# Optimization experiments

Hardware: AMD Instinct MI355X
Metric: run time of the kernel (lower is better)

## Reference

```python
import jax, jax.numpy as jnp
import numpy as np

C = 256
H = 8
D = C // H


def setup_inputs() -> dict:
    key = jax.random.key(0)
    ks = jax.random.split(key, 6)
    scale = 1.0 / np.sqrt(C)
    x = jax.random.normal(ks[0], (8, C, 2048), dtype=jnp.float32)
    Wq = jax.random.normal(ks[1], (C, C), dtype=jnp.float32) * scale
    Wk = jax.random.normal(ks[2], (C, C), dtype=jnp.float32) * scale
    Wv = jax.random.normal(ks[3], (C, C), dtype=jnp.float32) * scale
    Wo = jax.random.normal(ks[4], (C, C), dtype=jnp.float32) * scale
    bo = jax.random.normal(ks[5], (C,), dtype=jnp.float32) * 0.01
    return {"x": x, "Wq": Wq, "Wk": Wk, "Wv": Wv, "Wo": Wo, "bo": bo}


def reference(x, Wq, Wk, Wv, Wo, bo):
    # x: [N, C, L]; Conv1d(k=1) == per-position matmul with weight [out, in]
    q = jnp.einsum('oc,ncl->nol', Wq, x)
    k = jnp.einsum('oc,ncl->nol', Wk, x)
    v = jnp.einsum('oc,ncl->nol', Wv, x)
    N, _, L = x.shape
    # rearrange 'n (h d) l -> n l h d'
    q = q.reshape(N, H, D, L).transpose(0, 3, 1, 2)
    k = k.reshape(N, H, D, L).transpose(0, 3, 1, 2)
    v = v.reshape(N, H, D, L).transpose(0, 3, 1, 2)
    qk = jnp.einsum('nqhd,nkhd->nhqk', q, k)
    # NOTE: original scales by full embedding size (channels), not head_dim
    attn = jax.nn.softmax(qk * (C ** -0.5), axis=3)
    out = jnp.einsum('nhql,nlhd->nqhd', attn, v)
    # rearrange 'n l h d -> n (h d) l'
    out = out.transpose(0, 2, 3, 1).reshape(N, C, L)
    return jnp.einsum('oc,ncl->nol', Wo, out) + bo[None, :, None]
```

## Files before the change

### kernel.cpp

```cpp
#include <hip/hip_runtime.h>


typedef __bf16 bf8 __attribute__((ext_vector_type(8)));
typedef float f4 __attribute__((ext_vector_type(4)));
typedef float f32x4 __attribute__((ext_vector_type(4)));
typedef unsigned short u16;
typedef unsigned int u32;
typedef u16 u16x4 __attribute__((ext_vector_type(4)));
typedef u16 u16x8 __attribute__((ext_vector_type(8)));

__device__ __forceinline__ u16 f2bf(float f) {
  __bf16 h = (__bf16)f;
  return __builtin_bit_cast(u16, h);
}
__device__ __forceinline__ u32 pk2bf(float a, float b) {
  return ((u32)f2bf(b) << 16) | (u32)f2bf(a);
}
__device__ __forceinline__ u32 pktrunc(float a, float b) {
  return __builtin_amdgcn_perm(__builtin_bit_cast(u32, b),
                               __builtin_bit_cast(u32, a), 0x07060302u);
}
__device__ __forceinline__ float exp2_fast(float x) {
  return __builtin_amdgcn_exp2f(x);
}

#define MFMA(a, b, c) __builtin_amdgcn_mfma_f32_16x16x32_bf16((a), (b), (c), 0, 0, 0)

union bf8u { u32 u[4]; bf8 v; };
__device__ __forceinline__ bf8 mkbf8(u32 a, u32 b, u32 c, u32 d) {
  bf8u t; t.u[0] = a; t.u[1] = b; t.u[2] = c; t.u[3] = d; return t.v;
}
__device__ __forceinline__ bf8 ldw8(const float* p) {
  f32x4 u = *(const f32x4*)p;
  f32x4 v = *(const f32x4*)(p + 4);
  return mkbf8(pk2bf(u[0], u[1]), pk2bf(u[2], u[3]),
               pk2bf(v[0], v[1]), pk2bf(v[2], v[3]));
}

__global__ __launch_bounds__(256) void qkv_proj(
    const float* __restrict__ x, const float* __restrict__ Wq,
    const float* __restrict__ Wk, const float* __restrict__ Wv,
    u16* __restrict__ qbuf, u16* __restrict__ kbuf, u16* __restrict__ vbuf) {
  __shared__ __align__(16) u16 xt[64 * 264];
  const int n = blockIdx.z;
  const int o0 = blockIdx.y * 64;
  const int l0 = blockIdx.x * 64;
  const int tid = threadIdx.x;
  const int w = tid >> 6, lane = tid & 63, quad = lane >> 4, l16 = lane & 15;
  const int ow = o0 + w * 16;
  const float SC = 0.09019327066650391f;

  const int cp2 = tid >> 4;
  const int lq = (tid & 15) * 4;
#pragma unroll
  for (int it = 0; it < 8; ++it) {
    const float* xp = x + (size_t)(n * 256 + it * 32 + 2 * cp2) * 2048 + l0 + lq;
    f32x4 r0 = *(const f32x4*)xp;
    f32x4 r1 = *(const f32x4*)(xp + 2048);
#pragma unroll
    for (int i = 0; i < 4; ++i)
      *(u32*)&xt[(lq + i) * 264 + it * 32 + 2 * cp2] = pk2bf(r0[i], r1[i]);
  }
  __syncthreads();

  f4 accq[4], acck[4], accv[4];
#pragma unroll
  for (int lt = 0; lt < 4; ++lt) {
    accq[lt] = (f4){0.f, 0.f, 0.f, 0.f};
    acck[lt] = (f4){0.f, 0.f, 0.f, 0.f};
    accv[lt] = (f4){0.f, 0.f, 0.f, 0.f};
  }

  const float* wqp = Wq + (ow + l16) * 256 + quad * 8;
  const float* wkp = Wk + (ow + l16) * 256 + quad * 8;
  const float* wvp = Wv + (ow + l16) * 256 + quad * 8;

#pragma unroll
  for (int s = 0; s < 8; ++s) {
    const int c0 = s * 32;
    bf8 a0 = ldw8(wqp + c0);
    bf8 a1 = ldw8(wkp + c0);
    bf8 a2 = ldw8(wvp + c0);
#pragma unroll
    for (int lt = 0; lt < 4; ++lt) {
      bf8 b = *(const bf8*)&xt[(lt * 16 + l16) * 264 + c0 + quad * 8];
      accq[lt] = MFMA(a0, b, accq[lt]);
      acck[lt] = MFMA(a1, b, acck[lt]);
      accv[lt] = MFMA(b, a2, accv[lt]);
    }
  }

  const int hh = ow >> 5;
  const int dbase = (ow & 31) + quad * 4;
#pragma unroll
  for (int lt = 0; lt < 4; ++lt) {
    const int l = l0 + lt * 16 + l16;
    const size_t base = ((size_t)(n * 8 + hh) * 2048 + l) * 32 + dbase;
    u16x4 qv, kv;
#pragma unroll
    for (int r = 0; r < 4; ++r) {
      qv[r] = f2bf(accq[lt][r] * SC);
      kv[r] = f2bf(acck[lt][r]);
    }
    *(u16x4*)(qbuf + base) = qv;
    *(u16x4*)(kbuf + base) = kv;
  }
#pragma unroll
  for (int g = 0; g < 2; ++g) {
    u16x8 vv;
#pragma unroll
    for (int r = 0; r < 4; ++r) {
      vv[r] = f2bf(accv[2 * g][r]);
      vv[4 + r] = f2bf(accv[2 * g + 1][r]);
    }
    *(u16x8*)(vbuf + ((size_t)(n * 256 + ow + l16)) * 2048 + l0 + g * 32 + quad * 8) = vv;
  }
}

__global__ __launch_bounds__(256) void attn(
    const u16* __restrict__ qbuf, const u16* __restrict__ kbuf,
    const u16* __restrict__ vbuf, u16* __restrict__ abuf) {
  __shared__ float Osh[3][64][37];
  const int head = blockIdx.x, qblk = blockIdx.y;
  const int n = head >> 3, h = head & 7;
  const int tid = threadIdx.x;
  const int w = tid >> 6, lane = tid & 63;
  const int quad = lane >> 4, l16 = lane & 15;
  const int q0 = qblk * 64;
  const int kc0 = w * 512;

  const u16* kb = kbuf + (size_t)head * 2048 * 32 + l16 * 32 + quad * 8;
  const u16* vb = vbuf + ((size_t)n * 256 + h * 32 + l16) * 2048 + quad * 8;

  const bf8 ones = mkbf8(0x3F803F80u, 0x3F803F80u, 0x3F803F80u, 0x3F803F80u);

  bf8 aq[4];
#pragma unroll
  for (int qt = 0; qt < 4; ++qt)
    aq[qt] = *(const bf8*)(qbuf + ((size_t)head * 2048 + q0 + qt * 16 + l16) * 32 + quad * 8);

  f4 O[2][4];
  f4 Lacc[4];
#pragma unroll
  for (int qt = 0; qt < 4; ++qt) {
    O[0][qt] = (f4){0.f, 0.f, 0.f, 0.f};
    O[1][qt] = (f4){0.f, 0.f, 0.f, 0.f};
    Lacc[qt] = (f4){0.f, 0.f, 0.f, 0.f};
  }

  bf8 bk[4], vf[4];
#pragma unroll
  for (int kt = 0; kt < 4; ++kt) bk[kt] = *(const bf8*)(kb + (kc0 + kt * 16) * 32);
#pragma unroll
  for (int dt = 0; dt < 2; ++dt)
#pragma unroll
    for (int g = 0; g < 2; ++g)
      vf[dt * 2 + g] = *(const bf8*)(vb + dt * 16 * 2048 + kc0 + g * 32);

  for (int kc = kc0; kc < kc0 + 512; kc += 64) {
    const int kn = (kc < kc0 + 448) ? kc + 64 : kc0;
    bf8 nk[4], nv[4];
#pragma unroll
    for (int kt = 0; kt < 4; ++kt) nk[kt] = *(const bf8*)(kb + (kn + kt * 16) * 32);
#pragma unroll
    for (int dt = 0; dt < 2; ++dt)
#pragma unroll
      for (int g = 0; g < 2; ++g)
        nv[dt * 2 + g] = *(const bf8*)(vb + dt * 16 * 2048 + kn + g * 32);

#pragma unroll
    for (int qt = 0; qt < 4; ++qt) {
      f4 z = (f4){0.f, 0.f, 0.f, 0.f};
      f4 s0 = MFMA(bk[0], aq[qt], z);
      f4 s1 = MFMA(bk[1], aq[qt], z);
      f4 s2 = MFMA(bk[2], aq[qt], z);
      f4 s3 = MFMA(bk[3], aq[qt], z);
      f4 e0, e1, e2, e3;
#pragma unroll
      for (int r = 0; r < 4; ++r) {
        e0[r] = exp2_fast(s0[r]);
        e1[r] = exp2_fast(s1[r]);
        e2[r] = exp2_fast(s2[r]);
        e3[r] = exp2_fast(s3[r]);
      }
      bf8 B0 = mkbf8(pktrunc(e0[0], e0[1]), pktrunc(e0[2], e0[3]),
                     pktrunc(e1[0], e1[1]), pktrunc(e1[2], e1[3]));
      bf8 B1 = mkbf8(pktrunc(e2[0], e2[1]), pktrunc(e2[2], e2[3]),
                     pktrunc(e3[0], e3[1]), pktrunc(e3[2], e3[3]));
      Lacc[qt] = MFMA(ones, B0, Lacc[qt]);
      Lacc[qt] = MFMA(ones, B1, Lacc[qt]);
#pragma unroll
      for (int dt = 0; dt < 2; ++dt) {
        f4 o = O[dt][qt];
        o = MFMA(vf[dt * 2 + 0], B0, o);
        o = MFMA(vf[dt * 2 + 1], B1, o);
        O[dt][qt] = o;
      }
    }
#pragma unroll
    for (int i = 0; i < 4; ++i) { bk[i] = nk[i]; vf[i] = nv[i]; }
  }

  if (w > 0) {
#pragma unroll
    for (int dt = 0; dt < 2; ++dt)
#pragma unroll
      for (int qt = 0; qt < 4; ++qt)
#pragma unroll
        for (int r = 0; r < 4; ++r)
          Osh[w - 1][lane][dt * 16 + qt * 4 + r] = O[dt][qt][r];
#pragma unroll
    for (int qt = 0; qt < 4; ++qt)
      Osh[w - 1][lane][32 + qt] = Lacc[qt][0];
  }
  __syncthreads();
  if (w == 0) {
#pragma unroll
    for (int p = 0; p < 3; ++p) {
#pragma unroll
      for (int dt = 0; dt < 2; ++dt)
#pragma unroll
        for (int qt = 0; qt < 4; ++qt)
#pragma unroll
          for (int r = 0; r < 4; ++r)
            O[dt][qt][r] += Osh[p][lane][dt * 16 + qt * 4 + r];
#pragma unroll
      for (int qt = 0; qt < 4; ++qt)
        Lacc[qt][0] += Osh[p][lane][32 + qt];
    }
#pragma unroll
    for (int qt = 0; qt < 4; ++qt) {
      const float inv = 1.0f / Lacc[qt][0];
      const int q = q0 + qt * 16 + l16;
#pragma unroll
      for (int dt = 0; dt < 2; ++dt) {
        u16x4 ov;
#pragma unroll
        for (int r = 0; r < 4; ++r) ov[r] = f2bf(O[dt][qt][r] * inv);
        *(u16x4*)(abuf + ((size_t)n * 2048 + q) * 256 + h * 32 + dt * 16 + quad * 4) = ov;
      }
    }
  }
}

__global__ __launch_bounds__(256) void out_proj(
    const u16* __restrict__ abuf, const float* __restrict__ Wo,
    const float* __restrict__ bo, float* __restrict__ out) {
  const int n = blockIdx.z;
  const int o0 = blockIdx.y * 64;
  const int l0 = blockIdx.x * 64;
  const int tid = threadIdx.x;
  const int w = tid >> 6, lane = tid & 63, quad = lane >> 4, l16 = lane & 15;
  const int ow = o0 + w * 16;

  const float* wp = Wo + (ow + l16) * 256 + quad * 8;
  const u16* ab = abuf + ((size_t)n * 2048 + l0 + l16) * 256 + quad * 8;

  f4 acc[4];
#pragma unroll
  for (int lt = 0; lt < 4; ++lt) acc[lt] = (f4){0.f, 0.f, 0.f, 0.f};

  f32x4 wa0 = *(const f32x4*)wp, wa1 = *(const f32x4*)(wp + 4);
  bf8 b[4];
#pragma unroll
  for (int lt = 0; lt < 4; ++lt) b[lt] = *(const bf8*)(ab + lt * 16 * 256);

  for (int c0 = 0; c0 < 256; c0 += 32) {
    const int cn = (c0 < 224) ? c0 + 32 : 0;
    f32x4 wn0 = *(const f32x4*)(wp + cn), wn1 = *(const f32x4*)(wp + cn + 4);
    bf8 nb[4];
#pragma unroll
    for (int lt = 0; lt < 4; ++lt)
      nb[lt] = *(const bf8*)(ab + lt * 16 * 256 + cn);
    bf8 a = mkbf8(pk2bf(wa0[0], wa0[1]), pk2bf(wa0[2], wa0[3]),
                  pk2bf(wa1[0], wa1[1]), pk2bf(wa1[2], wa1[3]));
#pragma unroll
    for (int lt = 0; lt < 4; ++lt) acc[lt] = MFMA(a, b[lt], acc[lt]);
    wa0 = wn0; wa1 = wn1;
#pragma unroll
    for (int lt = 0; lt < 4; ++lt) b[lt] = nb[lt];
  }
#pragma unroll
  for (int r = 0; r < 4; ++r) {
    const int o = ow + quad * 4 + r;
    const float bias = bo[o];
#pragma unroll
    for (int lt = 0; lt < 4; ++lt) {
      out[((size_t)n * 256 + o) * 2048 + l0 + lt * 16 + l16] = acc[lt][r] + bias;
    }
  }
}

extern "C" void kernel_launch(void* const* d_in, const int* in_sizes, int n_in,
                              void* d_out, int out_size, void* d_ws, size_t ws_size,
                              hipStream_t stream) {
  const float* x  = (const float*)d_in[0];
  const float* Wq = (const float*)d_in[1];
  const float* Wk = (const float*)d_in[2];
  const float* Wv = (const float*)d_in[3];
  const float* Wo = (const float*)d_in[4];
  const float* bo = (const float*)d_in[5];
  float* out = (float*)d_out;

  u16* ws = (u16*)d_ws;
  u16* qbuf = ws;
  u16* kbuf = qbuf + 4194304;
  u16* vbuf = kbuf + 4194304;
  u16* abuf = vbuf + 4194304;

  qkv_proj<<<dim3(32, 4, 8), 256, 0, stream>>>(x, Wq, Wk, Wv,
                                               qbuf, kbuf, vbuf);
  attn<<<dim3(64, 32), 256, 0, stream>>>(qbuf, kbuf, vbuf, abuf);
  out_proj<<<dim3(32, 4, 8), 256, 0, stream>>>(abuf, Wo, bo, out);
}
```

Baseline: 183.8 us.

## Double-buffer x staging in QKV projection and compute softmax sum without MFMA

The QKV projection now stages x through two small 32-channel shared-memory buffers, converting one chunk while computing on the previous one. The full 64x256 tile is no longer loaded upfront, which shrinks LDS use and adds a barrier per step. In attention, the row-sum MFMAs against a ones vector are replaced by scalar adds of the exp values plus cross-lane shuffles, and the K/V register prefetch is dropped. The cross-wave reduction is split into two smaller shared-memory passes to cut LDS footprint at the cost of extra barriers.

```diff
diff --git a/kernel.cpp b/kernel.cpp
--- a/kernel.cpp
+++ b/kernel.cpp
@@ -41,7 +41,7 @@
     const float* __restrict__ x, const float* __restrict__ Wq,
     const float* __restrict__ Wk, const float* __restrict__ Wv,
     u16* __restrict__ qbuf, u16* __restrict__ kbuf, u16* __restrict__ vbuf) {
-  __shared__ __align__(16) u16 xt[64 * 264];
+  __shared__ __align__(16) u16 xt[2][64 * 40];
   const int n = blockIdx.z;
   const int o0 = blockIdx.y * 64;
   const int l0 = blockIdx.x * 64;
@@ -50,19 +50,6 @@
   const int ow = o0 + w * 16;
   const float SC = 0.09019327066650391f;
 
-  const int cp2 = tid >> 4;
-  const int lq = (tid & 15) * 4;
-#pragma unroll
-  for (int it = 0; it < 8; ++it) {
-    const float* xp = x + (size_t)(n * 256 + it * 32 + 2 * cp2) * 2048 + l0 + lq;
-    f32x4 r0 = *(const f32x4*)xp;
-    f32x4 r1 = *(const f32x4*)(xp + 2048);
-#pragma unroll
-    for (int i = 0; i < 4; ++i)
-      *(u32*)&xt[(lq + i) * 264 + it * 32 + 2 * cp2] = pk2bf(r0[i], r1[i]);
-  }
-  __syncthreads();
-
   f4 accq[4], acck[4], accv[4];
 #pragma unroll
   for (int lt = 0; lt < 4; ++lt) {
@@ -71,19 +58,34 @@
     accv[lt] = (f4){0.f, 0.f, 0.f, 0.f};
   }
 
+  const int cp = tid >> 4;
+  const int lq = (tid & 15) * 4;
+
+  auto stage = [&](int c0, int buf) {
+    const float* xp = x + (n * 256 + c0 + 2 * cp) * 2048 + l0 + lq;
+    f32x4 r0 = *(const f32x4*)xp;
+    f32x4 r1 = *(const f32x4*)(xp + 2048);
+#pragma unroll
+    for (int i = 0; i < 4; ++i)
+      *(u32*)&xt[buf][(lq + i) * 40 + 2 * cp] = pk2bf(r0[i], r1[i]);
+  };
+
   const float* wqp = Wq + (ow + l16) * 256 + quad * 8;
   const float* wkp = Wk + (ow + l16) * 256 + quad * 8;
   const float* wvp = Wv + (ow + l16) * 256 + quad * 8;
 
-#pragma unroll
+  stage(0, 0);
   for (int s = 0; s < 8; ++s) {
+    __syncthreads();
+    if (s < 7) stage((s + 1) * 32, (s + 1) & 1);
     const int c0 = s * 32;
     bf8 a0 = ldw8(wqp + c0);
     bf8 a1 = ldw8(wkp + c0);
     bf8 a2 = ldw8(wvp + c0);
+    const u16* xb = xt[s & 1];
 #pragma unroll
     for (int lt = 0; lt < 4; ++lt) {
-      bf8 b = *(const bf8*)&xt[(lt * 16 + l16) * 264 + c0 + quad * 8];
+      bf8 b = *(const bf8*)&xb[(lt * 16 + l16) * 40 + quad * 8];
       accq[lt] = MFMA(a0, b, accq[lt]);
       acck[lt] = MFMA(a1, b, acck[lt]);
       accv[lt] = MFMA(b, a2, accv[lt]);
@@ -120,7 +122,7 @@
 __global__ __launch_bounds__(256) void attn(
     const u16* __restrict__ qbuf, const u16* __restrict__ kbuf,
     const u16* __restrict__ vbuf, u16* __restrict__ abuf) {
-  __shared__ float Osh[3][64][37];
+  __shared__ float Osh[3][64][21];
   const int head = blockIdx.x, qblk = blockIdx.y;
   const int n = head >> 3, h = head & 7;
   const int tid = threadIdx.x;
@@ -132,41 +134,29 @@
   const u16* kb = kbuf + (size_t)head * 2048 * 32 + l16 * 32 + quad * 8;
   const u16* vb = vbuf + ((size_t)n * 256 + h * 32 + l16) * 2048 + quad * 8;
 
-  const bf8 ones = mkbf8(0x3F803F80u, 0x3F803F80u, 0x3F803F80u, 0x3F803F80u);
-
   bf8 aq[4];
 #pragma unroll
   for (int qt = 0; qt < 4; ++qt)
     aq[qt] = *(const bf8*)(qbuf + ((size_t)head * 2048 + q0 + qt * 16 + l16) * 32 + quad * 8);
 
   f4 O[2][4];
-  f4 Lacc[4];
+  float lsum[4];
 #pragma unroll
   for (int qt = 0; qt < 4; ++qt) {
     O[0][qt] = (f4){0.f, 0.f, 0.f, 0.f};
     O[1][qt] = (f4){0.f, 0.f, 0.f, 0.f};
-    Lacc[qt] = (f4){0.f, 0.f, 0.f, 0.f};
-  }
-
-  bf8 bk[4], vf[4];
-#pragma unroll
-  for (int kt = 0; kt < 4; ++kt) bk[kt] = *(const bf8*)(kb + (kc0 + kt * 16) * 32);
-#pragma unroll
-  for (int dt = 0; dt < 2; ++dt)
-#pragma unroll
-    for (int g = 0; g < 2; ++g)
-      vf[dt * 2 + g] = *(const bf8*)(vb + dt * 16 * 2048 + kc0 + g * 32);
+    lsum[qt] = 0.f;
+  }
 
   for (int kc = kc0; kc < kc0 + 512; kc += 64) {
-    const int kn = (kc < kc0 + 448) ? kc + 64 : kc0;
-    bf8 nk[4], nv[4];
-#pragma unroll
-    for (int kt = 0; kt < 4; ++kt) nk[kt] = *(const bf8*)(kb + (kn + kt * 16) * 32);
+    bf8 bk[4], vf[4];
+#pragma unroll
+    for (int kt = 0; kt < 4; ++kt) bk[kt] = *(const bf8*)(kb + (kc + kt * 16) * 32);
 #pragma unroll
     for (int dt = 0; dt < 2; ++dt)
 #pragma unroll
       for (int g = 0; g < 2; ++g)
-        nv[dt * 2 + g] = *(const bf8*)(vb + dt * 16 * 2048 + kn + g * 32);
+        vf[dt * 2 + g] = *(const bf8*)(vb + dt * 16 * 2048 + kc + g * 32);
 
 #pragma unroll
     for (int qt = 0; qt < 4; ++qt) {
@@ -183,12 +173,13 @@
         e2[r] = exp2_fast(s2[r]);
         e3[r] = exp2_fast(s3[r]);
       }
+      f4 t01 = e0 + e1, t23 = e2 + e3;
+      f4 t = t01 + t23;
+      lsum[qt] += (t[0] + t[1]) + (t[2] + t[3]);
       bf8 B0 = mkbf8(pktrunc(e0[0], e0[1]), pktrunc(e0[2], e0[3]),
                      pktrunc(e1[0], e1[1]), pktrunc(e1[2], e1[3]));
       bf8 B1 = mkbf8(pktrunc(e2[0], e2[1]), pktrunc(e2[2], e2[3]),
                      pktrunc(e3[0], e3[1]), pktrunc(e3[2], e3[3]));
-      Lacc[qt] = MFMA(ones, B0, Lacc[qt]);
-      Lacc[qt] = MFMA(ones, B1, Lacc[qt]);
 #pragma unroll
       for (int dt = 0; dt < 2; ++dt) {
         f4 o = O[dt][qt];
@@ -197,40 +188,59 @@
         O[dt][qt] = o;
       }
     }
-#pragma unroll
-    for (int i = 0; i < 4; ++i) { bk[i] = nk[i]; vf[i] = nv[i]; }
+  }
+
+#pragma unroll
+  for (int qt = 0; qt < 4; ++qt) {
+    float s = lsum[qt];
+    s += __shfl_xor(s, 16);
+    s += __shfl_xor(s, 32);
+    lsum[qt] = s;
   }
 
   if (w > 0) {
 #pragma unroll
-    for (int dt = 0; dt < 2; ++dt)
-#pragma unroll
-      for (int qt = 0; qt < 4; ++qt)
-#pragma unroll
-        for (int r = 0; r < 4; ++r)
-          Osh[w - 1][lane][dt * 16 + qt * 4 + r] = O[dt][qt][r];
-#pragma unroll
-    for (int qt = 0; qt < 4; ++qt)
-      Osh[w - 1][lane][32 + qt] = Lacc[qt][0];
+    for (int qt = 0; qt < 4; ++qt) {
+#pragma unroll
+      for (int r = 0; r < 4; ++r)
+        Osh[w - 1][lane][qt * 4 + r] = O[0][qt][r];
+      Osh[w - 1][lane][16 + qt] = lsum[qt];
+    }
   }
   __syncthreads();
   if (w == 0) {
 #pragma unroll
     for (int p = 0; p < 3; ++p) {
 #pragma unroll
-      for (int dt = 0; dt < 2; ++dt)
-#pragma unroll
-        for (int qt = 0; qt < 4; ++qt)
-#pragma unroll
-          for (int r = 0; r < 4; ++r)
-            O[dt][qt][r] += Osh[p][lane][dt * 16 + qt * 4 + r];
+      for (int qt = 0; qt < 4; ++qt) {
+#pragma unroll
+        for (int r = 0; r < 4; ++r)
+          O[0][qt][r] += Osh[p][lane][qt * 4 + r];
+        lsum[qt] += Osh[p][lane][16 + qt];
+      }
+    }
+  }
+  __syncthreads();
+  if (w > 0) {
+#pragma unroll
+    for (int qt = 0; qt < 4; ++qt)
+#pragma unroll
+      for (int r = 0; r < 4; ++r)
+        Osh[w - 1][lane][qt * 4 + r] = O[1][qt][r];
+  }
+  __syncthreads();
+  if (w == 0) {
+#pragma unroll
+    for (int p = 0; p < 3; ++p)
 #pragma unroll
       for (int qt = 0; qt < 4; ++qt)
-        Lacc[qt][0] += Osh[p][lane][32 + qt];
-    }
+#pragma unroll
+        for (int r = 0; r < 4; ++r)
+          O[1][qt][r] += Osh[p][lane][qt * 4 + r];
+
 #pragma unroll
     for (int qt = 0; qt < 4; ++qt) {
-      const float inv = 1.0f / Lacc[qt][0];
+      const float inv = 1.0f / lsum[qt];
       const int q = q0 + qt * 16 + l16;
 #pragma unroll
       for (int dt = 0; dt < 2; ++dt) {
```

New measurement: 181.3 us. No clear change (-1.4%).
